# Performance work log

Hardware: AMD Instinct MI355X
Metric: run time of the kernel (lower is better)

## Reference

```python
import jax, jax.numpy as jnp
import numpy as np

QK_NOPE = 128  # qk_nope_head_dim; softmax scale uses nope+rope head dim
EPS = 1e-6

def _rmsnorm(x, w):
    return x * jax.lax.rsqrt(jnp.mean(x * x, axis=-1, keepdims=True) + EPS) * w

def _deinterleave(x):
    # torch: view(..., d//2, 2).transpose(-1, -2).reshape(..., d)
    return jnp.concatenate([x[..., 0::2], x[..., 1::2]], axis=-1)

def _rotate_half(x):
    h = x.shape[-1] // 2
    return jnp.concatenate([-x[..., h:], x[..., :h]], axis=-1)

def _rope_cos_sin(position_ids, dim, theta=10000.0):
    inv_freq = 1.0 / (theta ** (jnp.arange(0, dim, 2, dtype=jnp.float32) / dim))  # [dim/2]
    freqs = position_ids.astype(jnp.float32)[..., None] * inv_freq               # [B,S,dim/2]
    emb = jnp.concatenate([freqs, freqs], axis=-1)                               # [B,S,dim]
    return jnp.cos(emb)[:, None], jnp.sin(emb)[:, None]                          # [B,1,S,dim]


def setup_inputs() -> dict:
    B, S, HID, H = 2, 1024, 4096, 32
    QL, KVL, ROPE, V = 1536, 512, 64, 128
    key = jax.random.key(0)
    ks = jax.random.split(key, 8)
    def w(k, shape, fan_in):
        return jax.random.normal(k, shape, jnp.float32) * (fan_in ** -0.5)
    hidden_states = jax.random.normal(ks[0], (B, S, HID), jnp.float32)
    causal = jnp.tril(jnp.ones((S, S), bool))
    attention_mask = jnp.where(causal, 0.0, -1e9).astype(jnp.float32)[None, None]  # [1,1,S,S]
    position_ids = jnp.broadcast_to(jnp.arange(S, dtype=jnp.int32), (B, S))
    return {
        'hidden_states': hidden_states,
        'attention_mask': attention_mask,
        'position_ids': position_ids,
        'w_q_a': w(ks[1], (HID, QL), HID),
        'q_a_ln_w': jnp.ones((QL,), jnp.float32),
        'q_rope': w(ks[2], (QL, H * ROPE), QL),
        'fusedqk': w(ks[3], (H, QL, KVL), QL),
        'w_kv_a': w(ks[4], (HID, KVL + ROPE), HID),
        'kv_a_ln_w': jnp.ones((KVL,), jnp.float32),
        'per_head_v_up': w(ks[5], (H, KVL, V), KVL),
        'w_o': w(ks[6], (H * V, HID), H * V),
    }


def _mla_forward(hidden_states, attention_mask, position_ids, w_q_a, q_a_ln_w,
                 q_rope, fusedqk, w_kv_a, kv_a_ln_w, per_head_v_up, w_o):
    B, S, _ = hidden_states.shape
    H, QL, KVL = fusedqk.shape
    ROPE = q_rope.shape[1] // H
    # compressed KV projection (MQA): split into latent kv and rope key part
    ckv = hidden_states @ w_kv_a                              # [B,S,KVL+ROPE]
    kva = _rmsnorm(ckv[..., :KVL], kv_a_ln_w)                 # [B,S,KVL]
    k_pe = ckv[..., KVL:][:, None]                            # [B,1,S,ROPE]
    # low-rank query
    q_a = _rmsnorm(hidden_states @ w_q_a, q_a_ln_w)           # [B,S,QL]
    q_pe = (q_a @ q_rope).reshape(B, S, H, ROPE).transpose(0, 2, 1, 3)  # [B,H,S,ROPE]
    # interleaved RoPE (deinterleave then standard rotate-half)
    cos, sin = _rope_cos_sin(position_ids, ROPE)
    qd = _deinterleave(q_pe)
    kd = _deinterleave(k_pe)
    q_pe = qd * cos + _rotate_half(qd) * sin                  # [B,H,S,ROPE]
    k_pe = kd * cos + _rotate_half(kd) * sin                  # [B,1,S,ROPE]
    # absorbed query: q_a @ (q_up @ k_up^T), precomputed as fusedqk
    q_abs = jnp.einsum('bsr,hrc->bhsc', q_a, fusedqk)         # [B,H,S,KVL]
    query = jnp.concatenate([q_abs, q_pe], axis=-1)           # [B,H,S,KVL+ROPE]
    keys = jnp.concatenate([kva, k_pe[:, 0]], axis=-1)        # [B,S,KVL+ROPE]
    scale = (QK_NOPE + ROPE) ** -0.5
    scores = jnp.einsum('bhsd,btd->bhst', query, keys) * scale + attention_mask
    attn = jax.nn.softmax(scores, axis=-1)                    # [B,H,S,S]
    ctx = jnp.einsum('bhst,btc->bhsc', attn, kva)             # [B,H,S,KVL]
    out = jnp.einsum('bhsc,hcv->bhsv', ctx, per_head_v_up)    # [B,H,S,V]
    out = out.transpose(0, 2, 1, 3).reshape(B, S, -1)         # [B,S,H*V]
    return out @ w_o                                          # [B,S,HID]


def reference(hidden_states, attention_mask, position_ids, w_q_a, q_a_ln_w,
              q_rope, fusedqk, w_kv_a, kv_a_ln_w, per_head_v_up, w_o):
    return _mla_forward(hidden_states, attention_mask, position_ids, w_q_a,
                        q_a_ln_w, q_rope, fusedqk, w_kv_a, kv_a_ln_w,
                        per_head_v_up, w_o)
```

## Files before the change

### kernel.cpp

```cpp
#include <hip/hip_runtime.h>


typedef __attribute__((ext_vector_type(8))) short s16x8;
typedef __attribute__((ext_vector_type(4))) float f32x4;

__device__ __forceinline__ float bf2f(unsigned short u) {
  union { unsigned int i; float f; } v; v.i = ((unsigned int)u) << 16; return v.f;
}
__device__ __forceinline__ unsigned short f2bf(float f) {
  union { float f; unsigned int i; } v; v.f = f;
  unsigned int x = v.i;
  x += 0x7fffu + ((x >> 16) & 1u);
  return (unsigned short)(x >> 16);
}

__device__ __forceinline__ void async16(const unsigned short* g, unsigned short* l) {
  __builtin_amdgcn_global_load_lds(
      (const __attribute__((address_space(1))) unsigned int*)g,
      (__attribute__((address_space(3))) unsigned int*)l, 16, 0, 0);
}

__global__ __launch_bounds__(256) void conv_bf16(
    const float* __restrict__ s, unsigned short* __restrict__ d)
{
  const long long i = ((long long)blockIdx.x * 256 + threadIdx.x) * 8;
  float4 a = *(const float4*)(s + i);
  float4 b = *(const float4*)(s + i + 4);
  union { uint4 v; unsigned short u[8]; } o;
  o.u[0] = f2bf(a.x); o.u[1] = f2bf(a.y); o.u[2] = f2bf(a.z); o.u[3] = f2bf(a.w);
  o.u[4] = f2bf(b.x); o.u[5] = f2bf(b.y); o.u[6] = f2bf(b.z); o.u[7] = f2bf(b.w);
  *(uint4*)(d + i) = o.v;
}

__global__ __launch_bounds__(256) void transpose_w(
    const float* __restrict__ src, unsigned short* __restrict__ dst,
    int R, int C, long long sS, long long sD)
{
  __shared__ unsigned short tile[32][36];
  src += (long long)blockIdx.z * sS;
  dst += (long long)blockIdx.z * sD;
  const int c0 = blockIdx.x * 32, r0 = blockIdx.y * 32;
  const int tid = threadIdx.x;
  const int rr = tid >> 3, cc4 = (tid & 7) * 4;
  if (c0 < C) {
    float4 v = *(const float4*)(src + (long long)(r0 + rr) * C + c0 + cc4);
    tile[cc4 + 0][rr] = f2bf(v.x); tile[cc4 + 1][rr] = f2bf(v.y);
    tile[cc4 + 2][rr] = f2bf(v.z); tile[cc4 + 3][rr] = f2bf(v.w);
  } else {
#pragma unroll
    for (int j = 0; j < 4; ++j) tile[cc4 + j][rr] = 0;
  }
  __syncthreads();
  const int cr = tid >> 3, rc4 = (tid & 7) * 4;
  union { uint2 v; unsigned short u[4]; } o;
#pragma unroll
  for (int j = 0; j < 4; ++j) o.u[j] = tile[cr][rc4 + j];
  *(uint2*)(dst + (long long)(c0 + cr) * R + r0 + rc4) = o.v;
}

template<int ODT>
__global__ __launch_bounds__(256) void gemm128(
    const unsigned short* __restrict__ A, const unsigned short* __restrict__ Bt,
    void* __restrict__ Cv, int K, int lda, int ldb, int ldc, int batH,
    long long sAb, long long sAh, long long sBb, long long sBh,
    long long sCb, long long sCh)
{
  const int z = blockIdx.z;
  const int bz = z / batH, hz = z % batH;
  A  += (long long)bz * sAb + (long long)hz * sAh;
  Bt += (long long)bz * sBb + (long long)hz * sBh;
  const long long co = (long long)bz * sCb + (long long)hz * sCh;

  __shared__ __align__(16) unsigned short As[128 * 32];
  __shared__ __align__(16) unsigned short Bs[128 * 32];

  const int tid = threadIdx.x, w = tid >> 6, lane = tid & 63;
  const int quad = lane >> 4, ml = lane & 15;
  const int wm = (w >> 1) * 64, wn = (w & 1) * 64;
  const int m0 = blockIdx.y * 128, n0 = blockIdx.x * 128;

  const int r0 = tid >> 2, k8 = (tid & 3) * 8;
  const unsigned short* Ag0 = A  + (long long)(m0 + r0)      * lda + k8;
  const unsigned short* Ag1 = A  + (long long)(m0 + r0 + 64) * lda + k8;
  const unsigned short* Bg0 = Bt + (long long)(n0 + r0)      * ldb + k8;
  const unsigned short* Bg1 = Bt + (long long)(n0 + r0 + 64) * ldb + k8;
  unsigned short* la0 = &As[tid * 8];
  unsigned short* la1 = &As[(tid + 256) * 8];
  unsigned short* lb0 = &Bs[tid * 8];
  unsigned short* lb1 = &Bs[(tid + 256) * 8];

  f32x4 acc[4][4] = {};

  for (int k0 = 0; k0 < K; k0 += 32) {
    __syncthreads();
    async16(Ag0 + k0, la0);
    async16(Ag1 + k0, la1);
    async16(Bg0 + k0, lb0);
    async16(Bg1 + k0, lb1);
    __syncthreads();

    s16x8 af[4], bf[4];
#pragma unroll
    for (int mi = 0; mi < 4; ++mi)
      af[mi] = *(const s16x8*)(&As[(wm + mi * 16 + ml) * 32 + quad * 8]);
#pragma unroll
    for (int ni = 0; ni < 4; ++ni)
      bf[ni] = *(const s16x8*)(&Bs[(wn + ni * 16 + ml) * 32 + quad * 8]);
#pragma unroll
    for (int mi = 0; mi < 4; ++mi)
#pragma unroll
      for (int ni = 0; ni < 4; ++ni)
        acc[mi][ni] = __builtin_amdgcn_mfma_f32_16x16x32_bf16(af[mi], bf[ni], acc[mi][ni], 0, 0, 0);
  }

#pragma unroll
  for (int mi = 0; mi < 4; ++mi)
#pragma unroll
    for (int ni = 0; ni < 4; ++ni)
#pragma unroll
      for (int r = 0; r < 4; ++r) {
        const int row = m0 + wm + mi * 16 + quad * 4 + r;
        const int col = n0 + wn + ni * 16 + ml;
        if (ODT)
          ((unsigned short*)Cv)[co + (long long)row * ldc + col] = f2bf(acc[mi][ni][r]);
        else
          ((float*)Cv)[co + (long long)row * ldc + col] = acc[mi][ni][r];
      }
}

__global__ __launch_bounds__(256) void kv_norm_rope(
    const float* __restrict__ ckv, const float* __restrict__ w,
    const int* __restrict__ pos_ids, unsigned short* __restrict__ keys)
{
  __shared__ float sbuf[4];
  const int r = blockIdx.x, tid = threadIdx.x;
  const float* row = ckv + (long long)r * 640;
  float x0 = row[tid], x1 = row[256 + tid];
  float ss = x0 * x0 + x1 * x1;
#pragma unroll
  for (int o = 32; o; o >>= 1) ss += __shfl_xor(ss, o);
  if ((tid & 63) == 0) sbuf[tid >> 6] = ss;
  __syncthreads();
  const float tot = sbuf[0] + sbuf[1] + sbuf[2] + sbuf[3];
  const float rms = rsqrtf(tot / 512.0f + 1e-6f);
  unsigned short* kr = keys + (long long)r * 576;
  kr[tid]       = f2bf(x0 * rms * w[tid]);
  kr[256 + tid] = f2bf(x1 * rms * w[256 + tid]);
  if (tid < 32) {
    const float pos = (float)pos_ids[r];
    const float invf = exp2f(-0.41524101186098287f * (float)tid);
    float sn, c; sincosf(pos * invf, &sn, &c);
    const float a0 = row[512 + 2 * tid], a1 = row[512 + 2 * tid + 1];
    kr[512 + tid] = f2bf(a0 * c - a1 * sn);
    kr[544 + tid] = f2bf(a1 * c + a0 * sn);
  }
}

__global__ __launch_bounds__(256) void q_norm(
    const float* __restrict__ qa_f32, const float* __restrict__ w,
    unsigned short* __restrict__ qa_bf)
{
  __shared__ float sbuf[4];
  const int r = blockIdx.x, tid = threadIdx.x;
  const float* row = qa_f32 + (long long)r * 1536;
  float x[6]; float ss = 0.f;
#pragma unroll
  for (int j = 0; j < 6; ++j) { x[j] = row[tid + 256 * j]; ss += x[j] * x[j]; }
#pragma unroll
  for (int o = 32; o; o >>= 1) ss += __shfl_xor(ss, o);
  if ((tid & 63) == 0) sbuf[tid >> 6] = ss;
  __syncthreads();
  const float tot = sbuf[0] + sbuf[1] + sbuf[2] + sbuf[3];
  const float rms = rsqrtf(tot / 1536.0f + 1e-6f);
#pragma unroll
  for (int j = 0; j < 6; ++j) {
    const int idx = tid + 256 * j;
    qa_bf[(long long)r * 1536 + idx] = f2bf(x[j] * rms * w[idx]);
  }
}

__global__ __launch_bounds__(256) void rope_q(
    const unsigned short* __restrict__ qpe, const int* __restrict__ pos_ids,
    unsigned short* __restrict__ query)
{
  const int r = blockIdx.x;
  const int b = r >> 10, s = r & 1023;
  const float pos = (float)pos_ids[r];
  for (int p = threadIdx.x; p < 1024; p += 256) {
    const int h = p >> 5, i = p & 31;
    const float invf = exp2f(-0.41524101186098287f * (float)i);
    float sn, c; sincosf(pos * invf, &sn, &c);
    const float a0 = bf2f(qpe[(long long)r * 2048 + h * 64 + 2 * i]);
    const float a1 = bf2f(qpe[(long long)r * 2048 + h * 64 + 2 * i + 1]);
    const long long qrow = ((long long)(b * 32 + h) * 1024 + s) * 576;
    query[qrow + 512 + i] = f2bf(a0 * c - a1 * sn);
    query[qrow + 544 + i] = f2bf(a1 * c + a0 * sn);
  }
}

__global__ __launch_bounds__(256) void transpose_keys(
    const unsigned short* __restrict__ keys, unsigned short* __restrict__ keysT)
{
  __shared__ unsigned short tile[32][36];
  const int tid = threadIdx.x;
  const int t0 = blockIdx.x * 32, d0 = blockIdx.y * 32, b = blockIdx.z;
  const int r = tid >> 3, c4 = (tid & 7) * 4;
  *(uint2*)(&tile[r][c4]) =
      *(const uint2*)(keys + ((long long)(b * 1024 + t0 + r) * 576 + d0 + c4));
  __syncthreads();
  unsigned short v[4];
#pragma unroll
  for (int j = 0; j < 4; ++j) v[j] = tile[c4 + j][r];
  *(uint2*)(keysT + ((long long)(b * 512 + d0 + r) * 1024 + t0 + c4)) = *(uint2*)v;
}

__global__ __launch_bounds__(256, 2) void flash_mfma(
    const unsigned short* __restrict__ query,
    const unsigned short* __restrict__ keys,
    const unsigned short* __restrict__ keysT,
    unsigned short* __restrict__ ctx)
{
  __shared__ __align__(16) unsigned short Ks[32 * 576];
  __shared__ __align__(16) unsigned short Ps[4][640];
  __shared__ float alpha_s[64];
  __shared__ float l_s[64];
  __shared__ __align__(16) int rflag[4];

  const int tid = threadIdx.x, w = tid >> 6, lane = tid & 63;
  const int quad = lane >> 4, ml = lane & 15;
  const int bid = blockIdx.x;
  const int bh = bid & 63;
  const int qt = 15 - (bid >> 6);
  const int q0 = qt * 64;
  const int b = bh >> 5;
  const float scale = 0.07216878364870323f;

  const unsigned short* kb  = keys  + (long long)b * 1024 * 576;
  const unsigned short* vtb = keysT + (long long)b * 512 * 1024;

  const unsigned short* qg =
      query + ((long long)bh * 1024 + q0 + w * 16 + ml) * 576 + quad * 8;
  s16x8 qf[18];
#pragma unroll
  for (int ks = 0; ks < 18; ++ks) qf[ks] = *(const s16x8*)(qg + ks * 32);

  auto stageK = [&](int t0) {
#pragma unroll
    for (int i = 0; i < 9; ++i) {
      const int idx = i * 256 + tid;
      const int row = idx / 72;
      const int c16 = idx - row * 72;
      async16(kb + (long long)(t0 + row) * 576 + ((c16 ^ (row & 7)) << 3),
              &Ks[idx * 8]);
    }
  };

  const int e3 = ml & 7;
  const int qi = q0 + w * 16 + ml;
  const int ntile = 2 * qt + 2;

  float m = -1e30f, l = 0.f;
  f32x4 o[4][8] = {};

  stageK(0);
  __syncthreads();

  for (int ti = 0; ti < ntile; ++ti) {
    const int t0 = ti * 32;

    f32x4 sc0 = {}, sc1 = {};
#pragma unroll
    for (int ks = 0; ks < 18; ++ks) {
      const int xr = ((ks * 4 + quad) ^ e3) << 3;
      s16x8 k0 = *(const s16x8*)(&Ks[ml * 576 + xr]);
      s16x8 k1 = *(const s16x8*)(&Ks[ml * 576 + xr + 16 * 576]);
      sc0 = __builtin_amdgcn_mfma_f32_16x16x32_bf16(k0, qf[ks], sc0, 0, 0, 0);
      sc1 = __builtin_amdgcn_mfma_f32_16x16x32_bf16(k1, qf[ks], sc1, 0, 0, 0);
    }

    float p[8]; float mx = -1e30f;
    const bool tail = (ti >= ntile - 2);
#pragma unroll
    for (int r = 0; r < 4; ++r) {
      float v0 = sc0[r] * scale, v1 = sc1[r] * scale;
      if (tail) {
        if (t0 + quad * 4 + r > qi)      v0 = -1e30f;
        if (t0 + 16 + quad * 4 + r > qi) v1 = -1e30f;
      }
      p[r] = v0; p[4 + r] = v1;
      mx = fmaxf(mx, fmaxf(v0, v1));
    }
    mx = fmaxf(mx, __shfl_xor(mx, 16));
    mx = fmaxf(mx, __shfl_xor(mx, 32));

    float alpha = 1.0f;
    int resc = 0;
    if (!__all(mx - m <= 8.0f)) {
      const float mn = fmaxf(m, mx);
      alpha = __expf(m - mn);
      m = mn;
      l *= alpha;
      resc = 1;
    }
    if (lane == 0) rflag[w] = resc;
    if (quad == 0) alpha_s[w * 16 + ml] = alpha;

    float ps = 0.f;
#pragma unroll
    for (int j = 0; j < 8; ++j) { p[j] = __expf(p[j] - m); ps += p[j]; }
    ps += __shfl_xor(ps, 16);
    ps += __shfl_xor(ps, 32);
    l += ps;

#pragma unroll
    for (int c = 0; c < 2; ++c) {
      union { unsigned short u[4]; uint2 v; } pk;
      pk.u[0] = f2bf(p[c * 4 + 0]); pk.u[1] = f2bf(p[c * 4 + 1]);
      pk.u[2] = f2bf(p[c * 4 + 2]); pk.u[3] = f2bf(p[c * 4 + 3]);
      *(uint2*)(&Ps[w][ml * 40 + c * 16 + quad * 4]) = pk.v;
    }
    __syncthreads();

    if (ti + 1 < ntile) stageK(t0 + 32);

    s16x8 pa[4];
#pragma unroll
    for (int qc = 0; qc < 4; ++qc)
      pa[qc] = *(const s16x8*)(&Ps[qc][ml * 40 + quad * 8]);

    const int4 rf = *(const int4*)rflag;
    if (rf.x | rf.y | rf.z | rf.w) {
#pragma unroll
      for (int qc = 0; qc < 4; ++qc)
#pragma unroll
        for (int r = 0; r < 4; ++r) {
          const float a = alpha_s[qc * 16 + quad * 4 + r];
#pragma unroll
          for (int nt = 0; nt < 8; ++nt) o[qc][nt][r] *= a;
        }
    }

    const unsigned short* vg =
        vtb + (long long)(w * 128 + ml) * 1024 + t0 + quad * 8;
#pragma unroll
    for (int nt = 0; nt < 8; ++nt) {
      s16x8 vf = *(const s16x8*)(vg + nt * 16 * 1024);
#pragma unroll
      for (int qc = 0; qc < 4; ++qc)
        o[qc][nt] = __builtin_amdgcn_mfma_f32_16x16x32_bf16(pa[qc], vf, o[qc][nt], 0, 0, 0);
    }
    __syncthreads();
  }

  if (quad == 0) l_s[w * 16 + ml] = l;
  __syncthreads();

  unsigned short* cb = ctx + ((long long)bh * 1024 + q0) * 512 + w * 128 + ml;
#pragma unroll
  for (int qc = 0; qc < 4; ++qc)
#pragma unroll
    for (int r = 0; r < 4; ++r) {
      const float linv = 1.0f / l_s[qc * 16 + quad * 4 + r];
      unsigned short* crow = cb + (long long)(qc * 16 + quad * 4 + r) * 512;
#pragma unroll
      for (int nt = 0; nt < 8; ++nt)
        crow[nt * 16] = f2bf(o[qc][nt][r] * linv);
    }
}

extern "C" void kernel_launch(void* const* d_in, const int* in_sizes, int n_in,
                              void* d_out, int out_size, void* d_ws, size_t ws_size,
                              hipStream_t stream)
{
  (void)in_sizes; (void)n_in; (void)out_size; (void)ws_size;
  const float* hs      = (const float*)d_in[0];
  const int*   pos     = (const int*)d_in[2];
  const float* w_q_a   = (const float*)d_in[3];
  const float* q_a_ln  = (const float*)d_in[4];
  const float* q_rope  = (const float*)d_in[5];
  const float* fusedqk = (const float*)d_in[6];
  const float* w_kv_a  = (const float*)d_in[7];
  const float* kv_ln   = (const float*)d_in[8];
  const float* v_up    = (const float*)d_in[9];
  const float* w_o     = (const float*)d_in[10];
  char* ws = (char*)d_ws;

  unsigned short* woT    = (unsigned short*)(ws + 0);
  unsigned short* vupT   = (unsigned short*)(ws + 33554432);
  unsigned short* keys   = (unsigned short*)(ws + 37748736);
  unsigned short* keysT  = (unsigned short*)(ws + 40108032);
  unsigned short* ctx    = (unsigned short*)(ws + 42205184);
  unsigned short* fqkT   = (unsigned short*)(ws + 42205184);
  unsigned short* qab    = (unsigned short*)(ws + 92536832);
  unsigned short* qpe    = (unsigned short*)(ws + 99828288);
  unsigned short* hsb    = (unsigned short*)(ws + 92536832);
  unsigned short* query  = (unsigned short*)(ws + 109314048);
  unsigned short* wqT    = (unsigned short*)(ws + 109314048);
  unsigned short* wkvT   = (unsigned short*)(ws + 121896960);
  unsigned short* qropeT = (unsigned short*)(ws + 127139840);
  float*          ckv    = (float*)(ws + 133431296);
  float*          qaf    = (float*)(ws + 138674176);
  unsigned short* outh   = (unsigned short*)(ws + 109314048);

  const dim3 blk(256);

  conv_bf16<<<dim3(4096), blk, 0, stream>>>(hs, hsb);
  transpose_w<<<dim3(20, 128, 1), blk, 0, stream>>>(w_kv_a, wkvT, 4096, 576, 0, 0);
  transpose_w<<<dim3(48, 128, 1), blk, 0, stream>>>(w_q_a, wqT, 4096, 1536, 0, 0);
  transpose_w<<<dim3(64, 48, 1), blk, 0, stream>>>(q_rope, qropeT, 1536, 2048, 0, 0);
  transpose_w<<<dim3(16, 48, 32), blk, 0, stream>>>(fusedqk, fqkT, 1536, 512,
      (long long)1536 * 512, (long long)512 * 1536);
  transpose_w<<<dim3(4, 16, 32), blk, 0, stream>>>(v_up, vupT, 512, 128,
      (long long)512 * 128, (long long)128 * 512);
  transpose_w<<<dim3(128, 128, 1), blk, 0, stream>>>(w_o, woT, 4096, 4096, 0, 0);

  gemm128<0><<<dim3(5, 16, 1), blk, 0, stream>>>(hsb, wkvT, (void*)ckv,
      4096, 4096, 4096, 640, 1, 0, 0, 0, 0, 0, 0);
  kv_norm_rope<<<dim3(2048), blk, 0, stream>>>(ckv, kv_ln, pos, keys);
  transpose_keys<<<dim3(32, 16, 2), blk, 0, stream>>>(keys, keysT);
  gemm128<0><<<dim3(12, 16, 1), blk, 0, stream>>>(hsb, wqT, (void*)qaf,
      4096, 4096, 4096, 1536, 1, 0, 0, 0, 0, 0, 0);
  q_norm<<<dim3(2048), blk, 0, stream>>>(qaf, q_a_ln, qab);
  gemm128<1><<<dim3(16, 16, 1), blk, 0, stream>>>(qab, qropeT, (void*)qpe,
      1536, 1536, 1536, 2048, 1, 0, 0, 0, 0, 0, 0);
  rope_q<<<dim3(2048), blk, 0, stream>>>(qpe, pos, query);
  gemm128<1><<<dim3(4, 8, 64), blk, 0, stream>>>(qab, fqkT, (void*)query,
      1536, 1536, 1536, 576, 32,
      (long long)1024 * 1536, 0, 0, (long long)512 * 1536,
      (long long)32 * 1024 * 576, (long long)1024 * 576);
  flash_mfma<<<dim3(1024), blk, 0, stream>>>(query, keys, keysT, ctx);
  gemm128<1><<<dim3(1, 8, 64), blk, 0, stream>>>(ctx, vupT, (void*)outh,
      512, 512, 512, 4096, 32,
      (long long)32 * 1024 * 512, (long long)1024 * 512, 0, (long long)128 * 512,
      (long long)1024 * 4096, 128);
  gemm128<0><<<dim3(32, 16, 1), blk, 0, stream>>>(outh, woT, d_out,
      4096, 4096, 4096, 4096, 1, 0, 0, 0, 0, 0, 0);
}
```

Before: 1.051 ms.

## Double-buffer K tiles in flash attention with 512-thread blocks over 128-query tiles

The flash attention kernel now runs 8 waves per block over 128 query rows. Each block reuses one K tile across twice as many queries, and each wave owns 64 of the 512 context columns. K tiles are double-buffered in LDS with async loads issued one tile ahead and explicit vmcnt waits, replacing the old stage-then-sync pattern. Waves whose query rows are fully masked skip the score computation, and masked PV blocks are skipped. The costs are a larger LDS footprint, higher register pressure, and half as many blocks, which may hurt occupancy and load balance.

```diff
diff --git a/kernel.cpp b/kernel.cpp
--- a/kernel.cpp
+++ b/kernel.cpp
@@ -214,24 +214,24 @@
   *(uint2*)(keysT + ((long long)(b * 512 + d0 + r) * 1024 + t0 + c4)) = *(uint2*)v;
 }
 
-__global__ __launch_bounds__(256, 2) void flash_mfma(
+__global__ __launch_bounds__(512, 2) void flash_mfma(
     const unsigned short* __restrict__ query,
     const unsigned short* __restrict__ keys,
     const unsigned short* __restrict__ keysT,
     unsigned short* __restrict__ ctx)
 {
-  __shared__ __align__(16) unsigned short Ks[32 * 576];
-  __shared__ __align__(16) unsigned short Ps[4][640];
-  __shared__ float alpha_s[64];
-  __shared__ float l_s[64];
-  __shared__ __align__(16) int rflag[4];
+  __shared__ __align__(16) unsigned short Ks[2][32 * 640];
+  __shared__ __align__(16) unsigned short Ps[2][8][640];
+  __shared__ float alpha_s[2][128];
+  __shared__ float l_s[128];
+  __shared__ __align__(16) int rflag[2][8];
 
   const int tid = threadIdx.x, w = tid >> 6, lane = tid & 63;
   const int quad = lane >> 4, ml = lane & 15;
   const int bid = blockIdx.x;
   const int bh = bid & 63;
-  const int qt = 15 - (bid >> 6);
-  const int q0 = qt * 64;
+  const int qt = 7 - (bid >> 6);
+  const int q0 = qt * 128;
   const int b = bh >> 5;
   const float scale = 0.07216878364870323f;
 
@@ -244,126 +244,151 @@
 #pragma unroll
   for (int ks = 0; ks < 18; ++ks) qf[ks] = *(const s16x8*)(qg + ks * 32);
 
-  auto stageK = [&](int t0) {
-#pragma unroll
-    for (int i = 0; i < 9; ++i) {
-      const int idx = i * 256 + tid;
-      const int row = idx / 72;
-      const int c16 = idx - row * 72;
-      async16(kb + (long long)(t0 + row) * 576 + ((c16 ^ (row & 7)) << 3),
-              &Ks[idx * 8]);
-    }
+  int koff[5];
+#pragma unroll
+  for (int j = 0; j < 5; ++j) {
+    const int idx = tid + 512 * j;
+    const int row = idx / 80;
+    const int c16 = idx - row * 80;
+    koff[j] = row * 576 + ((c16 ^ (row & 7)) << 3);
+  }
+  char* ldsb = (char*)&Ks[0][0] + tid * 16;
+  auto stage = [&](int t, int buf) {
+    const long long toff = (long long)t * 18432;
+    char* lb = ldsb + buf * 40960;
+#pragma unroll
+    for (int j = 0; j < 5; ++j)
+      async16(kb + toff + koff[j], (unsigned short*)(lb + j * 8192));
   };
 
   const int e3 = ml & 7;
   const int qi = q0 + w * 16 + ml;
-  const int ntile = 2 * qt + 2;
+  const int ntile = 4 * qt + 4;
 
   float m = -1e30f, l = 0.f;
-  f32x4 o[4][8] = {};
-
-  stageK(0);
-  __syncthreads();
+  f32x4 o[8][4] = {};
+
+  stage(0, 0);
 
   for (int ti = 0; ti < ntile; ++ti) {
+    const int buf = ti & 1;
     const int t0 = ti * 32;
 
-    f32x4 sc0 = {}, sc1 = {};
-#pragma unroll
-    for (int ks = 0; ks < 18; ++ks) {
-      const int xr = ((ks * 4 + quad) ^ e3) << 3;
-      s16x8 k0 = *(const s16x8*)(&Ks[ml * 576 + xr]);
-      s16x8 k1 = *(const s16x8*)(&Ks[ml * 576 + xr + 16 * 576]);
-      sc0 = __builtin_amdgcn_mfma_f32_16x16x32_bf16(k0, qf[ks], sc0, 0, 0, 0);
-      sc1 = __builtin_amdgcn_mfma_f32_16x16x32_bf16(k1, qf[ks], sc1, 0, 0, 0);
+    if (ti + 1 < ntile) {
+      stage(ti + 1, buf ^ 1);
+      asm volatile("s_waitcnt vmcnt(5)" ::: "memory");
+    } else {
+      asm volatile("s_waitcnt vmcnt(0)" ::: "memory");
     }
-
-    float p[8]; float mx = -1e30f;
-    const bool tail = (ti >= ntile - 2);
-#pragma unroll
-    for (int r = 0; r < 4; ++r) {
-      float v0 = sc0[r] * scale, v1 = sc1[r] * scale;
-      if (tail) {
-        if (t0 + quad * 4 + r > qi)      v0 = -1e30f;
-        if (t0 + 16 + quad * 4 + r > qi) v1 = -1e30f;
+    __builtin_amdgcn_sched_barrier(0);
+    __builtin_amdgcn_s_barrier();
+    __builtin_amdgcn_sched_barrier(0);
+
+    const bool wdead = (t0 > q0 + w * 16 + 15);
+    if (!wdead) {
+      const unsigned short* Kb = &Ks[buf][0];
+      f32x4 sc0 = {}, sc1 = {};
+#pragma unroll
+      for (int ks = 0; ks < 18; ++ks) {
+        const int xr = ((ks * 4 + quad) ^ e3) << 3;
+        s16x8 k0 = *(const s16x8*)(Kb + ml * 640 + xr);
+        s16x8 k1 = *(const s16x8*)(Kb + (16 + ml) * 640 + xr);
+        sc0 = __builtin_amdgcn_mfma_f32_16x16x32_bf16(k0, qf[ks], sc0, 0, 0, 0);
+        sc1 = __builtin_amdgcn_mfma_f32_16x16x32_bf16(k1, qf[ks], sc1, 0, 0, 0);
       }
-      p[r] = v0; p[4 + r] = v1;
-      mx = fmaxf(mx, fmaxf(v0, v1));
+
+      float p[8]; float mx = -1e30f;
+      const bool tail = (t0 + 31 > q0 + w * 16);
+#pragma unroll
+      for (int r = 0; r < 4; ++r) {
+        float v0 = sc0[r] * scale, v1 = sc1[r] * scale;
+        if (tail) {
+          if (t0 + quad * 4 + r > qi)      v0 = -1e30f;
+          if (t0 + 16 + quad * 4 + r > qi) v1 = -1e30f;
+        }
+        p[r] = v0; p[4 + r] = v1;
+        mx = fmaxf(mx, fmaxf(v0, v1));
+      }
+      mx = fmaxf(mx, __shfl_xor(mx, 16));
+      mx = fmaxf(mx, __shfl_xor(mx, 32));
+
+      float alpha = 1.0f;
+      int resc = 0;
+      if (!__all(mx - m <= 8.0f)) {
+        const float mn = fmaxf(m, mx);
+        alpha = __expf(m - mn);
+        m = mn;
+        l *= alpha;
+        resc = 1;
+      }
+      if (lane == 0) rflag[buf][w] = resc;
+      if (quad == 0) alpha_s[buf][w * 16 + ml] = alpha;
+
+      float ps = 0.f;
+#pragma unroll
+      for (int j = 0; j < 8; ++j) { p[j] = __expf(p[j] - m); ps += p[j]; }
+      ps += __shfl_xor(ps, 16);
+      ps += __shfl_xor(ps, 32);
+      l += ps;
+
+#pragma unroll
+      for (int c = 0; c < 2; ++c) {
+        union { unsigned short u[4]; uint2 v; } pk;
+        pk.u[0] = f2bf(p[c * 4 + 0]); pk.u[1] = f2bf(p[c * 4 + 1]);
+        pk.u[2] = f2bf(p[c * 4 + 2]); pk.u[3] = f2bf(p[c * 4 + 3]);
+        *(uint2*)(&Ps[buf][w][ml * 40 + c * 16 + quad * 4]) = pk.v;
+      }
+    } else {
+      if (lane == 0) rflag[buf][w] = 0;
+      if (quad == 0) alpha_s[buf][w * 16 + ml] = 1.0f;
     }
-    mx = fmaxf(mx, __shfl_xor(mx, 16));
-    mx = fmaxf(mx, __shfl_xor(mx, 32));
-
-    float alpha = 1.0f;
-    int resc = 0;
-    if (!__all(mx - m <= 8.0f)) {
-      const float mn = fmaxf(m, mx);
-      alpha = __expf(m - mn);
-      m = mn;
-      l *= alpha;
-      resc = 1;
-    }
-    if (lane == 0) rflag[w] = resc;
-    if (quad == 0) alpha_s[w * 16 + ml] = alpha;
-
-    float ps = 0.f;
-#pragma unroll
-    for (int j = 0; j < 8; ++j) { p[j] = __expf(p[j] - m); ps += p[j]; }
-    ps += __shfl_xor(ps, 16);
-    ps += __shfl_xor(ps, 32);
-    l += ps;
-
-#pragma unroll
-    for (int c = 0; c < 2; ++c) {
-      union { unsigned short u[4]; uint2 v; } pk;
-      pk.u[0] = f2bf(p[c * 4 + 0]); pk.u[1] = f2bf(p[c * 4 + 1]);
-      pk.u[2] = f2bf(p[c * 4 + 2]); pk.u[3] = f2bf(p[c * 4 + 3]);
-      *(uint2*)(&Ps[w][ml * 40 + c * 16 + quad * 4]) = pk.v;
-    }
-    __syncthreads();
-
-    if (ti + 1 < ntile) stageK(t0 + 32);
-
-    s16x8 pa[4];
-#pragma unroll
-    for (int qc = 0; qc < 4; ++qc)
-      pa[qc] = *(const s16x8*)(&Ps[qc][ml * 40 + quad * 8]);
-
-    const int4 rf = *(const int4*)rflag;
-    if (rf.x | rf.y | rf.z | rf.w) {
-#pragma unroll
-      for (int qc = 0; qc < 4; ++qc)
+
+    const unsigned short* vg =
+        vtb + (long long)(w * 64 + ml) * 1024 + t0 + quad * 8;
+    s16x8 vf[4];
+#pragma unroll
+    for (int nt = 0; nt < 4; ++nt) vf[nt] = *(const s16x8*)(vg + nt * 16 * 1024);
+
+    asm volatile("s_waitcnt lgkmcnt(0)" ::: "memory");
+    __builtin_amdgcn_sched_barrier(0);
+    __builtin_amdgcn_s_barrier();
+    __builtin_amdgcn_sched_barrier(0);
+
+    const int4 ra = *(const int4*)&rflag[buf][0];
+    const int4 rb = *(const int4*)&rflag[buf][4];
+    if (ra.x | ra.y | ra.z | ra.w | rb.x | rb.y | rb.z | rb.w) {
+#pragma unroll
+      for (int qc = 0; qc < 8; ++qc)
 #pragma unroll
         for (int r = 0; r < 4; ++r) {
-          const float a = alpha_s[qc * 16 + quad * 4 + r];
-#pragma unroll
-          for (int nt = 0; nt < 8; ++nt) o[qc][nt][r] *= a;
+          const float a = alpha_s[buf][qc * 16 + quad * 4 + r];
+#pragma unroll
+          for (int nt = 0; nt < 4; ++nt) o[qc][nt][r] *= a;
         }
     }
 
-    const unsigned short* vg =
-        vtb + (long long)(w * 128 + ml) * 1024 + t0 + quad * 8;
-#pragma unroll
-    for (int nt = 0; nt < 8; ++nt) {
-      s16x8 vf = *(const s16x8*)(vg + nt * 16 * 1024);
-#pragma unroll
-      for (int qc = 0; qc < 4; ++qc)
-        o[qc][nt] = __builtin_amdgcn_mfma_f32_16x16x32_bf16(pa[qc], vf, o[qc][nt], 0, 0, 0);
+#pragma unroll
+    for (int qc = 0; qc < 8; ++qc) {
+      if (t0 > q0 + qc * 16 + 15) continue;
+      s16x8 pa = *(const s16x8*)(&Ps[buf][qc][ml * 40 + quad * 8]);
+#pragma unroll
+      for (int nt = 0; nt < 4; ++nt)
+        o[qc][nt] = __builtin_amdgcn_mfma_f32_16x16x32_bf16(pa, vf[nt], o[qc][nt], 0, 0, 0);
     }
-    __syncthreads();
   }
 
   if (quad == 0) l_s[w * 16 + ml] = l;
   __syncthreads();
 
-  unsigned short* cb = ctx + ((long long)bh * 1024 + q0) * 512 + w * 128 + ml;
-#pragma unroll
-  for (int qc = 0; qc < 4; ++qc)
+  unsigned short* cb = ctx + ((long long)bh * 1024 + q0) * 512 + w * 64 + ml;
+#pragma unroll
+  for (int qc = 0; qc < 8; ++qc)
 #pragma unroll
     for (int r = 0; r < 4; ++r) {
       const float linv = 1.0f / l_s[qc * 16 + quad * 4 + r];
       unsigned short* crow = cb + (long long)(qc * 16 + quad * 4 + r) * 512;
 #pragma unroll
-      for (int nt = 0; nt < 8; ++nt)
+      for (int nt = 0; nt < 4; ++nt)
         crow[nt * 16] = f2bf(o[qc][nt][r] * linv);
     }
 }
@@ -428,7 +453,7 @@
       1536, 1536, 1536, 576, 32,
       (long long)1024 * 1536, 0, 0, (long long)512 * 1536,
       (long long)32 * 1024 * 576, (long long)1024 * 576);
-  flash_mfma<<<dim3(1024), blk, 0, stream>>>(query, keys, keysT, ctx);
+  flash_mfma<<<dim3(512), dim3(512), 0, stream>>>(query, keys, keysT, ctx);
   gemm128<1><<<dim3(1, 8, 64), blk, 0, stream>>>(ctx, vupT, (void*)outh,
       512, 512, 512, 4096, 32,
       (long long)32 * 1024 * 512, (long long)1024 * 512, 0, (long long)128 * 512,
```

Result: faster. 1.009 ms (-4.0%).
